# Performance work log

Measured on AMD Instinct MI355X. Metric: run time of the kernel, lower is better.

Reference implementation:

```python
import jax, jax.numpy as jnp
import numpy as np
import math
from jax import lax

D_MODEL = 128
N_HEADS = 8
D_HEAD = D_MODEL // N_HEADS
D_FF = 4 * D_MODEL
KERNEL = 25  # moving_avg kernel size
N_LAYERS = 2
EPS = 1e-5


def moving_avg(x):
    # x: [B, L, D]; replicate-pad (KERNEL-1)//2 at both ends, window mean (AvgPool1d stride 1)
    p = (KERNEL - 1) // 2
    xp = jnp.concatenate([jnp.repeat(x[:, :1], p, axis=1), x, jnp.repeat(x[:, -1:], p, axis=1)], axis=1)
    s = lax.reduce_window(xp, 0.0, lax.add, (1, KERNEL, 1), (1, 1, 1), 'VALID')
    return s / KERNEL


def series_decomp(x):
    mm = moving_avg(x)
    return x - mm, mm


def autocorrelation(q, k, v):
    # q,k,v: [B, L, H, E]; FFT-based period correlation + top-k time-delay aggregation (training path)
    B, L, H, E = q.shape
    top_k = int(1 * math.log(L))  # factor=1
    qf = jnp.fft.rfft(q.transpose(0, 2, 3, 1), axis=-1)
    kf = jnp.fft.rfft(k.transpose(0, 2, 3, 1), axis=-1)
    corr = jnp.fft.irfft(qf * jnp.conj(kf), n=L, axis=-1)  # [B, H, E, L]
    vals = v.transpose(0, 2, 3, 1)                          # [B, H, E, L]
    mean_value = corr.mean(axis=(1, 2))                     # [B, L]
    _, index = lax.top_k(mean_value.mean(axis=0), top_k)    # [top_k], lags shared over batch
    weights = mean_value[:, index]                          # [B, top_k]
    tmp_corr = jax.nn.softmax(weights, axis=-1)
    agg = jnp.zeros_like(vals)
    for i in range(top_k):  # static small loop (top_k = 8)
        pattern = jnp.roll(vals, -index[i], axis=-1)
        agg = agg + pattern * tmp_corr[:, i][:, None, None, None]
    return agg.transpose(0, 3, 1, 2)  # [B, L, H, E]


def attn_layer(x, w, b):
    # w: [4, D, D] (q,k,v,out torch-Linear weights), b: [4, D]
    B, L, D = x.shape
    q = (jnp.einsum('bld,ed->ble', x, w[0]) + b[0]).reshape(B, L, N_HEADS, D_HEAD)
    k = (jnp.einsum('bld,ed->ble', x, w[1]) + b[1]).reshape(B, L, N_HEADS, D_HEAD)
    v = (jnp.einsum('bld,ed->ble', x, w[2]) + b[2]).reshape(B, L, N_HEADS, D_HEAD)
    o = autocorrelation(q, k, v).reshape(B, L, D)
    return jnp.einsum('bld,ed->ble', o, w[3]) + b[3]


def encoder_layer(x, w, b, w1, w2):
    x = x + attn_layer(x, w, b)
    x, _ = series_decomp(x)
    y = jax.nn.gelu(jnp.einsum('bld,fd->blf', x, w1), approximate=False)  # conv1 (k=1, no bias)
    y = jnp.einsum('blf,df->bld', y, w2)                                   # conv2 (k=1, no bias)
    res, _ = series_decomp(x + y)
    return res


def reference(x_enc, emb_w, attn_w, attn_b, ffn_w1, ffn_w2, norm_g, norm_b, fc1_w, fc1_b, fc2_w, fc2_b):
    # token embedding: Conv1d(C -> D, kernel 3, circular padding, no bias)
    xc = x_enc.transpose(0, 2, 1)  # [B, C, L]
    xc = jnp.concatenate([xc[:, :, -1:], xc, xc[:, :, :1]], axis=-1)
    h = lax.conv_general_dilated(xc, emb_w, (1,), 'VALID', dimension_numbers=('NCH', 'OIH', 'NCH'))
    h = h.transpose(0, 2, 1)  # [B, L, D]
    for l in range(N_LAYERS):
        h = encoder_layer(h, attn_w[l], attn_b[l], ffn_w1[l], ffn_w2[l])
    # my_Layernorm: LayerNorm then subtract time-mean
    mu = h.mean(axis=-1, keepdims=True)
    var = ((h - mu) ** 2).mean(axis=-1, keepdims=True)
    ln = (h - mu) / jnp.sqrt(var + EPS) * norm_g + norm_b
    h = ln - ln.mean(axis=1, keepdims=True)
    # head: gelu -> mean pool over time -> MLP
    h = jax.nn.gelu(h, approximate=False).mean(axis=1)  # [B, D]
    h = jax.nn.relu(jnp.einsum('bd,hd->bh', h, fc1_w) + fc1_b)
    return jnp.einsum('bh,ch->bc', h, fc2_w) + fc2_b


def setup_inputs() -> dict:
    key = jax.random.key(0)
    ks = jax.random.split(key, 8)
    B, L, C, NC, FC = 32, 4096, 12, 5, 128
    s = 0.02
    return {
        'x_enc': jax.random.normal(ks[0], (B, L, C), jnp.float32),
        'emb_w': jax.random.normal(ks[1], (D_MODEL, C, 3), jnp.float32) * s,
        'attn_w': jax.random.normal(ks[2], (N_LAYERS, 4, D_MODEL, D_MODEL), jnp.float32) * s,
        'attn_b': jnp.zeros((N_LAYERS, 4, D_MODEL), jnp.float32),
        'ffn_w1': jax.random.normal(ks[3], (N_LAYERS, D_FF, D_MODEL), jnp.float32) * s,
        'ffn_w2': jax.random.normal(ks[4], (N_LAYERS, D_MODEL, D_FF), jnp.float32) * s,
        'norm_g': jnp.ones((D_MODEL,), jnp.float32),
        'norm_b': jnp.zeros((D_MODEL,), jnp.float32),
        'fc1_w': jax.random.normal(ks[5], (FC, D_MODEL), jnp.float32) * s,
        'fc1_b': jnp.zeros((FC,), jnp.float32),
        'fc2_w': jax.random.normal(ks[6], (NC, FC), jnp.float32) * s,
        'fc2_b': jnp.zeros((NC,), jnp.float32),
    }
```

## Files before the change

kernel.cpp:

```cpp
#include <hip/hip_runtime.h>
#include <math.h>

#define L_SEQ 4096
#define BATCH 32
#define DM 128

typedef short short8 __attribute__((ext_vector_type(8)));
typedef float f32x4 __attribute__((ext_vector_type(4)));

__device__ __forceinline__ float gelu_f(float x) {
    return 0.5f * x * (1.0f + erff(x * 0.70710678118654752f));
}
__device__ __forceinline__ float gelu_fast(float x) {
    float ax = fabsf(x);
    if (ax < 1.0f) {
        float z = x * 0.70710678118654752f;
        float z2 = z * z;
        float p = 1.0f + z2 * (-0.333333333f + z2 * (0.1f + z2 * (-0.0238095238f +
                  z2 * (4.62962963e-3f + z2 * (-7.57575758e-4f)))));
        return 0.5f * x * (1.0f + 1.1283791670955126f * z * p);
    }
    return 0.5f * x * (1.0f + erff(x * 0.70710678118654752f));
}
__device__ __forceinline__ unsigned short f2b(float f) {
    unsigned u = __float_as_uint(f);
    u += 0x7fffu + ((u >> 16) & 1u);
    return (unsigned short)(u >> 16);
}
__device__ __forceinline__ float b2f(unsigned short h) {
    return __uint_as_float(((unsigned)h) << 16);
}

__global__ __launch_bounds__(256) void kembed(const float* __restrict__ x,
                                              const float* __restrict__ w,
                                              float* __restrict__ h) {
    __shared__ float xs[130][12];
    __shared__ float wsm[128][37];
    int b = blockIdx.x >> 5;
    int lt = blockIdx.x & 31;
    int l0 = lt * 128;
    int tid = threadIdx.x;
    for (int i = tid; i < 130 * 12; i += 256) {
        int r = i / 12, c = i - r * 12;
        int gl = (l0 - 1 + r + 4096) & 4095;
        xs[r][c] = x[((size_t)b * 4096 + gl) * 12 + c];
    }
    for (int i = tid; i < 128 * 36; i += 256) {
        int o = i / 36, j = i - o * 36;
        wsm[o][j] = w[i];
    }
    __syncthreads();
    int o = tid & 127, lh = tid >> 7;
    float wr[36];
#pragma unroll
    for (int j = 0; j < 36; j++) wr[j] = wsm[o][j];
    int base_r = lh * 64;
    float ring[4][12];
#pragma unroll
    for (int c = 0; c < 12; c++) { ring[0][c] = xs[base_r][c]; ring[1][c] = xs[base_r + 1][c]; }
    float* hp = h + ((size_t)b * 4096 + l0 + lh * 64) * 128 + o;
#pragma unroll 4
    for (int st = 0; st < 64; st++) {
        int s0 = st & 3, s1 = (st + 1) & 3, s2 = (st + 2) & 3;
#pragma unroll
        for (int c = 0; c < 12; c++) ring[s2][c] = xs[base_r + st + 2][c];
        float s = 0.f;
#pragma unroll
        for (int c = 0; c < 12; c++)
            s += wr[c * 3 + 0] * ring[s0][c] + wr[c * 3 + 1] * ring[s1][c] + wr[c * 3 + 2] * ring[s2][c];
        hp[(size_t)st * 128] = s;
    }
}

__global__ __launch_bounds__(256) void kprepw(const float* __restrict__ w1,
                                              const float* __restrict__ w2,
                                              unsigned short* __restrict__ w1img,
                                              unsigned short* __restrict__ w2img) {
    int t = blockIdx.x * 256 + threadIdx.x;
    int layer = t >> 17; int rem = t & 131071;
    if (rem < 65536) {
        int R = rem >> 7, x = rem & 127;
        int g = x >> 3, j = x & 7;
        int srcc = ((g ^ (R & 7)) << 3) + j;
        w1img[(size_t)layer * 65536 + rem] = f2b(w1[(size_t)layer * 65536 + R * 128 + srcc]);
    } else {
        int r2 = rem - 65536;
        int c = r2 >> 13; int D = (r2 >> 6) & 127; int x = r2 & 63;
        int g = x >> 3, j = x & 7;
        int srcf = c * 64 + ((g ^ (D & 7)) << 3) + j;
        w2img[(size_t)layer * 65536 + r2] = f2b(w2[(size_t)layer * 65536 + D * 512 + srcf]);
    }
}

__global__ __launch_bounds__(256, 2) void kgemm_qk3(const float* __restrict__ A,
                                                    const float* __restrict__ aw,
                                                    const float* __restrict__ ab,
                                                    int half, float* __restrict__ CT) {
    __shared__ __align__(16) char smem[65536];
    short* Ah = (short*)smem;
    short* Al = (short*)(smem + 16384);
    short* Wh = (short*)(smem + 32768);
    short* Wl = (short*)(smem + 49152);
    int y = blockIdx.y;
    const float* Wp = aw + (size_t)y * 16384 + (size_t)half * 64 * 128;
    const float* bias = ab + y * 128 + half * 64;
    int row0 = blockIdx.x * 64;
    int tid = threadIdx.x;
#pragma unroll
    for (int u = 0; u < 4; u++) {
        int task = tid + u * 256;
        int r = task >> 4, cg = task & 15;
        int dst = r * 128 + ((cg ^ (r & 7)) << 3);
        const float* src = A + ((size_t)(row0 + r)) * 128 + cg * 8;
        float4 xa = *(const float4*)src, ya = *(const float4*)(src + 4);
        float av[8] = {xa.x, xa.y, xa.z, xa.w, ya.x, ya.y, ya.z, ya.w};
        short8 hi, lo;
#pragma unroll
        for (int j = 0; j < 8; j++) {
            unsigned short h = f2b(av[j]);
            hi[j] = (short)h; lo[j] = (short)f2b(av[j] - b2f(h));
        }
        *(short8*)(Ah + dst) = hi; *(short8*)(Al + dst) = lo;
        const float* wsrc = Wp + (size_t)r * 128 + cg * 8;
        float4 xw = *(const float4*)wsrc, yw = *(const float4*)(wsrc + 4);
        float wv[8] = {xw.x, xw.y, xw.z, xw.w, yw.x, yw.y, yw.z, yw.w};
        short8 whi, wlo;
#pragma unroll
        for (int j = 0; j < 8; j++) {
            unsigned short h = f2b(wv[j]);
            whi[j] = (short)h; wlo[j] = (short)f2b(wv[j] - b2f(h));
        }
        *(short8*)(Wh + dst) = whi; *(short8*)(Wl + dst) = wlo;
    }
    __syncthreads();
    int l = tid & 63; int w = tid >> 6; int wm = w >> 1, wn = w & 1;
    f32x4 acc[2][2];
#pragma unroll
    for (int i = 0; i < 2; i++)
#pragma unroll
        for (int j = 0; j < 2; j++) acc[i][j] = (f32x4){0.f, 0.f, 0.f, 0.f};
#pragma unroll
    for (int ks = 0; ks < 4; ks++) {
        int cg = ks * 4 + (l >> 4);
        short8 ah[2], al2[2], bh[2], bl[2];
#pragma unroll
        for (int mi = 0; mi < 2; mi++) {
            int rm = wm * 32 + mi * 16 + (l & 15);
            int off = rm * 128 + ((cg ^ (rm & 7)) << 3);
            ah[mi] = *(short8*)(Ah + off); al2[mi] = *(short8*)(Al + off);
        }
#pragma unroll
        for (int ni = 0; ni < 2; ni++) {
            int rn = wn * 32 + ni * 16 + (l & 15);
            int off = rn * 128 + ((cg ^ (rn & 7)) << 3);
            bh[ni] = *(short8*)(Wh + off); bl[ni] = *(short8*)(Wl + off);
        }
#pragma unroll
        for (int mi = 0; mi < 2; mi++)
#pragma unroll
            for (int ni = 0; ni < 2; ni++) {
                acc[mi][ni] = __builtin_amdgcn_mfma_f32_16x16x32_bf16(ah[mi], bh[ni], acc[mi][ni], 0, 0, 0);
                acc[mi][ni] = __builtin_amdgcn_mfma_f32_16x16x32_bf16(ah[mi], bl[ni], acc[mi][ni], 0, 0, 0);
                acc[mi][ni] = __builtin_amdgcn_mfma_f32_16x16x32_bf16(al2[mi], bh[ni], acc[mi][ni], 0, 0, 0);
            }
    }
    __syncthreads();
    float* Dsh = (float*)smem;
#pragma unroll
    for (int mi = 0; mi < 2; mi++)
#pragma unroll
        for (int ni = 0; ni < 2; ni++)
#pragma unroll
            for (int rr = 0; rr < 4; rr++) {
                int m = wm * 32 + mi * 16 + (l >> 4) * 4 + rr;
                int n = wn * 32 + ni * 16 + (l & 15);
                Dsh[n * 68 + m] = acc[mi][ni][rr] + bias[n];
            }
    __syncthreads();
    int b = row0 >> 12; int l0 = row0 & 4095;
    int cbase = y * 64;
#pragma unroll
    for (int u = 0; u < 4; u++) {
        int task = tid + u * 256;
        int c = task >> 4, m4 = (task & 15) * 4;
        float4 v = *(float4*)&Dsh[c * 68 + m4];
        *(float4*)&CT[((size_t)(b * 128 + cbase + c)) * 4096 + l0 + m4] = v;
    }
}

template <int AT, int EPI>
__global__ __launch_bounds__(256, 2) void kgemm_mfma(const void* __restrict__ Ap,
                                                     const float* __restrict__ Wf,
                                                     const float* __restrict__ bias,
                                                     const float* __restrict__ res,
                                                     const float* __restrict__ tcb,
                                                     const int* __restrict__ idxb,
                                                     void* __restrict__ outp) {
    __shared__ __align__(16) char smem[65536];
    short* As = (short*)smem;
    short* Ws = (short*)(smem + 32768);
    int tid = threadIdx.x;
    size_t row0 = (size_t)blockIdx.x * 128;
#pragma unroll
    for (int u = 0; u < 8; u++) {
        int g = tid + u * 256;
        int r = g >> 4, cg = g & 15;
        int dsti = r * 128 + ((cg ^ (r & 7)) << 3);
        short8 v;
        if (AT == 0) {
            const float* src = (const float*)Ap + (row0 + r) * 128 + cg * 8;
            float4 x = *(const float4*)src, y = *(const float4*)(src + 4);
            v[0] = f2b(x.x); v[1] = f2b(x.y); v[2] = f2b(x.z); v[3] = f2b(x.w);
            v[4] = f2b(y.x); v[5] = f2b(y.y); v[6] = f2b(y.z); v[7] = f2b(y.w);
        } else if (AT == 1) {
            v = *(const short8*)((const short*)Ap + (row0 + r) * 128 + cg * 8);
        } else {
            const unsigned short* Vb = (const unsigned short*)Ap;
            int b = (int)(row0 >> 12);
            int l0 = (int)(row0 & 4095);
            float accv[8];
#pragma unroll
            for (int j = 0; j < 8; j++) accv[j] = 0.f;
#pragma unroll
            for (int i = 0; i < 8; i++) {
                float wgt = tcb[b * 8 + i];
                int lr = (l0 + r + idxb[i]) & 4095;
                short8 vv = *(const short8*)(Vb + ((size_t)(b * 4096 + lr)) * 128 + cg * 8);
#pragma unroll
                for (int j = 0; j < 8; j++) accv[j] += wgt * b2f((unsigned short)vv[j]);
            }
#pragma unroll
            for (int j = 0; j < 8; j++) v[j] = (short)f2b(accv[j]);
        }
        *(short8*)(As + dsti) = v;
        const float* ws = Wf + (size_t)r * 128 + cg * 8;
        float4 wx = *(const float4*)ws, wy = *(const float4*)(ws + 4);
        short8 wv;
        wv[0] = f2b(wx.x); wv[1] = f2b(wx.y); wv[2] = f2b(wx.z); wv[3] = f2b(wx.w);
        wv[4] = f2b(wy.x); wv[5] = f2b(wy.y); wv[6] = f2b(wy.z); wv[7] = f2b(wy.w);
        *(short8*)(Ws + dsti) = wv;
    }
    __syncthreads();
    int l = tid & 63; int w = tid >> 6; int wm = w >> 1, wn = w & 1;
    f32x4 acc[4][4];
#pragma unroll
    for (int i = 0; i < 4; i++)
#pragma unroll
        for (int j = 0; j < 4; j++) acc[i][j] = (f32x4){0.f, 0.f, 0.f, 0.f};
#pragma unroll
    for (int ks = 0; ks < 4; ks++) {
        int cg = ks * 4 + (l >> 4);
        short8 af[4], bf[4];
#pragma unroll
        for (int mi = 0; mi < 4; mi++) {
            int rm = wm * 64 + mi * 16 + (l & 15);
            af[mi] = *(short8*)(As + rm * 128 + ((cg ^ (rm & 7)) << 3));
        }
#pragma unroll
        for (int ni = 0; ni < 4; ni++) {
            int rn = wn * 64 + ni * 16 + (l & 15);
            bf[ni] = *(short8*)(Ws + rn * 128 + ((cg ^ (rn & 7)) << 3));
        }
#pragma unroll
        for (int mi = 0; mi < 4; mi++)
#pragma unroll
            for (int ni = 0; ni < 4; ni++)
                acc[mi][ni] = __builtin_amdgcn_mfma_f32_16x16x32_bf16(af[mi], bf[ni], acc[mi][ni], 0, 0, 0);
    }
    __syncthreads();
    float* Dsh = (float*)smem;
#pragma unroll
    for (int mi = 0; mi < 4; mi++)
#pragma unroll
        for (int ni = 0; ni < 4; ni++)
#pragma unroll
            for (int rr = 0; rr < 4; rr++)
                Dsh[(wm * 64 + mi * 16 + (l >> 4) * 4 + rr) * 128 + wn * 64 + ni * 16 + (l & 15)] = acc[mi][ni][rr];
    __syncthreads();
#pragma unroll
    for (int u = 0; u < 8; u++) {
        int g = tid + u * 256;
        int r = g >> 4, c8 = (g & 15) * 8;
        float vv[8];
#pragma unroll
        for (int j = 0; j < 8; j++) vv[j] = Dsh[r * 128 + c8 + j] + bias[c8 + j];
        if (EPI == 1) {
            const float* rp = res + (row0 + r) * 128 + c8;
#pragma unroll
            for (int j = 0; j < 8; j++) vv[j] += rp[j];
            float* op = (float*)outp + (row0 + r) * 128 + c8;
            *(float4*)op = make_float4(vv[0], vv[1], vv[2], vv[3]);
            *(float4*)(op + 4) = make_float4(vv[4], vv[5], vv[6], vv[7]);
        } else {
            short8 ov;
#pragma unroll
            for (int j = 0; j < 8; j++) ov[j] = (short)f2b(vv[j]);
            *(short8*)((short*)outp + (row0 + r) * 128 + c8) = ov;
        }
    }
}

__global__ __launch_bounds__(256, 2) void kffn_mfma(const float* __restrict__ xs,
                                                    const unsigned short* __restrict__ w1img,
                                                    const unsigned short* __restrict__ w2img,
                                                    float* __restrict__ outp) {
    __shared__ __align__(16) char smem[81920];
    short* xsl = (short*)smem;
    short* w1t = (short*)(smem + 32768);
    short* tt  = (short*)(smem + 49152);
    short* w2t = (short*)(smem + 65536);
    int tid = threadIdx.x;
    size_t row0 = (size_t)blockIdx.x * 128;
#pragma unroll
    for (int u = 0; u < 8; u++) {
        int g = tid + u * 256;
        int r = g >> 4, cg = g & 15;
        const float* src = xs + (row0 + r) * 128 + cg * 8;
        float4 x = *(const float4*)src, y = *(const float4*)(src + 4);
        short8 v;
        v[0] = f2b(x.x); v[1] = f2b(x.y); v[2] = f2b(x.z); v[3] = f2b(x.w);
        v[4] = f2b(y.x); v[5] = f2b(y.y); v[6] = f2b(y.z); v[7] = f2b(y.w);
        *(short8*)(xsl + r * 128 + ((cg ^ (r & 7)) << 3)) = v;
    }
    int l = tid & 63; int w = tid >> 6; int wm = w >> 1, wn = w & 1;
    f32x4 acc2[4][4];
#pragma unroll
    for (int i = 0; i < 4; i++)
#pragma unroll
        for (int j = 0; j < 4; j++) acc2[i][j] = (f32x4){0.f, 0.f, 0.f, 0.f};
    for (int fb = 0; fb < 8; fb++) {
        __syncthreads();
#pragma unroll
        for (int u = 0; u < 4; u++) {
            int task = tid + u * 256;
            int r = task >> 4, cg = task & 15;
            *(short8*)(w1t + r * 128 + cg * 8) =
                *(const short8*)(w1img + ((size_t)(fb * 64 + r)) * 128 + cg * 8);
            int r2 = task >> 3, cg2 = task & 7;
            *(short8*)(w2t + r2 * 64 + cg2 * 8) =
                *(const short8*)(w2img + ((size_t)(fb * 128 + r2)) * 64 + cg2 * 8);
        }
        __syncthreads();
        f32x4 a1[4][2];
#pragma unroll
        for (int i = 0; i < 4; i++)
#pragma unroll
            for (int j = 0; j < 2; j++) a1[i][j] = (f32x4){0.f, 0.f, 0.f, 0.f};
#pragma unroll
        for (int ks = 0; ks < 4; ks++) {
            int cg = ks * 4 + (l >> 4);
            short8 af[4], bf[2];
#pragma unroll
            for (int mi = 0; mi < 4; mi++) {
                int rm = wm * 64 + mi * 16 + (l & 15);
                af[mi] = *(short8*)(xsl + rm * 128 + ((cg ^ (rm & 7)) << 3));
            }
#pragma unroll
            for (int ni = 0; ni < 2; ni++) {
                int rn = wn * 32 + ni * 16 + (l & 15);
                bf[ni] = *(short8*)(w1t + rn * 128 + ((cg ^ (rn & 7)) << 3));
            }
#pragma unroll
            for (int mi = 0; mi < 4; mi++)
#pragma unroll
                for (int ni = 0; ni < 2; ni++)
                    a1[mi][ni] = __builtin_amdgcn_mfma_f32_16x16x32_bf16(af[mi], bf[ni], a1[mi][ni], 0, 0, 0);
        }
#pragma unroll
        for (int mi = 0; mi < 4; mi++)
#pragma unroll
            for (int ni = 0; ni < 2; ni++)
#pragma unroll
                for (int rr = 0; rr < 4; rr++) {
                    int m = wm * 64 + mi * 16 + (l >> 4) * 4 + rr;
                    int f = wn * 32 + ni * 16 + (l & 15);
                    tt[m * 64 + (((f >> 3) ^ (m & 7)) << 3) + (f & 7)] = (short)f2b(gelu_fast(a1[mi][ni][rr]));
                }
        __syncthreads();
#pragma unroll
        for (int ks = 0; ks < 2; ks++) {
            int cg = ks * 4 + (l >> 4);
            short8 af[4], bf[4];
#pragma unroll
            for (int mi = 0; mi < 4; mi++) {
                int rm = wm * 64 + mi * 16 + (l & 15);
                af[mi] = *(short8*)(tt + rm * 64 + ((cg ^ (rm & 7)) << 3));
            }
#pragma unroll
            for (int ni = 0; ni < 4; ni++) {
                int rn = wn * 64 + ni * 16 + (l & 15);
                bf[ni] = *(short8*)(w2t + rn * 64 + ((cg ^ (rn & 7)) << 3));
            }
#pragma unroll
            for (int mi = 0; mi < 4; mi++)
#pragma unroll
                for (int ni = 0; ni < 4; ni++)
                    acc2[mi][ni] = __builtin_amdgcn_mfma_f32_16x16x32_bf16(af[mi], bf[ni], acc2[mi][ni], 0, 0, 0);
        }
    }
    __syncthreads();
    float* Dsh = (float*)smem;
#pragma unroll
    for (int mi = 0; mi < 4; mi++)
#pragma unroll
        for (int ni = 0; ni < 4; ni++)
#pragma unroll
            for (int rr = 0; rr < 4; rr++)
                Dsh[(wm * 64 + mi * 16 + (l >> 4) * 4 + rr) * 128 + wn * 64 + ni * 16 + (l & 15)] = acc2[mi][ni][rr];
    __syncthreads();
#pragma unroll
    for (int u = 0; u < 8; u++) {
        int g = tid + u * 256;
        int r = g >> 4, c8 = (g & 15) * 8;
        const float* rp = xs + (row0 + r) * 128 + c8;
        float* op = outp + (row0 + r) * 128 + c8;
        float4 o0, o1;
        o0.x = Dsh[r * 128 + c8 + 0] + rp[0]; o0.y = Dsh[r * 128 + c8 + 1] + rp[1];
        o0.z = Dsh[r * 128 + c8 + 2] + rp[2]; o0.w = Dsh[r * 128 + c8 + 3] + rp[3];
        o1.x = Dsh[r * 128 + c8 + 4] + rp[4]; o1.y = Dsh[r * 128 + c8 + 5] + rp[5];
        o1.z = Dsh[r * 128 + c8 + 6] + rp[6]; o1.w = Dsh[r * 128 + c8 + 7] + rp[7];
        *(float4*)op = o0; *(float4*)(op + 4) = o1;
    }
}

#define FIDX(a) ((a) + ((a) >> 4))

__device__ __forceinline__ float2 twget(const float2* __restrict__ tw, int a, float sgn) {
    float2 T = tw[a & 1023];
    int hi = (a >> 10) & 3;
    float cs = (hi & 1) ? ((hi & 2) ? T.y : -T.y) : ((hi & 2) ? -T.x : T.x);
    float sn = (hi & 1) ? ((hi & 2) ? -T.x : T.x) : ((hi & 2) ? -T.y : T.y);
    return make_float2(cs, sn * sgn);
}

__device__ void fft4096_r4(float2* __restrict__ b0, float2* __restrict__ b1,
                           const float2* __restrict__ tw, float sgn, int tid) {
    float2* cur = b0; float2* nxt = b1;
#pragma unroll
    for (int t = 0; t < 6; t++) {
        int s = 1 << (t << 1);
        int q = tid & (s - 1);
        int ps = tid - q;
        float2 a0 = cur[FIDX(tid)];
        float2 a1 = cur[FIDX(tid + 1024)];
        float2 a2 = cur[FIDX(tid + 2048)];
        float2 a3 = cur[FIDX(tid + 3072)];
        float t0x = a0.x + a2.x, t0y = a0.y + a2.y;
        float t1x = a0.x - a2.x, t1y = a0.y - a2.y;
        float t2x = a1.x + a3.x, t2y = a1.y + a3.y;
        float t3x = a1.x - a3.x, t3y = a1.y - a3.y;
        float it3x = -sgn * t3y, it3y = sgn * t3x;
        float2 A0 = make_float2(t0x + t2x, t0y + t2y);
        float2 A1 = make_float2(t1x + it3x, t1y + it3y);
        float2 A2 = make_float2(t0x - t2x, t0y - t2y);
        float2 A3 = make_float2(t1x - it3x, t1y - it3y);
        int ob = q + (ps << 2);
        nxt[FIDX(ob)] = A0;
        float2 w1 = twget(tw, ps, sgn);
        float2 w2 = twget(tw, ps * 2, sgn);
        float2 w3 = twget(tw, ps * 3, sgn);
        nxt[FIDX(ob + s)] = make_float2(A1.x * w1.x - A1.y * w1.y, A1.x * w1.y + A1.y * w1.x);
        nxt[FIDX(ob + 2 * s)] = make_float2(A2.x * w2.x - A2.y * w2.y, A2.x * w2.y + A2.y * w2.x);
        nxt[FIDX(ob + 3 * s)] = make_float2(A3.x * w3.x - A3.y * w3.y, A3.x * w3.y + A3.y * w3.x);
        __syncthreads();
        float2* tp = cur; cur = nxt; nxt = tp;
    }
}

__global__ __launch_bounds__(1024) void kfft_fwd(const float* __restrict__ qkT,
                                                 float* __restrict__ Pws, int ghalf) {
    __shared__ float2 bufA[4352];
    __shared__ float2 bufB[4352];
    __shared__ float2 tw[1024];
    int tid = threadIdx.x;
    {
        float sn, cs;
        sincosf(1.5339807878856412e-3f * (float)tid, &sn, &cs);
        tw[tid] = make_float2(cs, sn);
    }
    int b = blockIdx.x >> 3;
    int gl = blockIdx.x & 7;
    float2 pacc[4];
#pragma unroll
    for (int j = 0; j < 4; j++) pacc[j] = make_float2(0.f, 0.f);
    for (int c8 = 0; c8 < 8; c8++) {
        int c = gl * 8 + c8;
        const float* qrow = qkT + ((size_t)(b * 128 + c)) * 4096;
        const float* krow = qkT + ((size_t)(b * 128 + 64 + c)) * 4096;
        __syncthreads();
#pragma unroll
        for (int j = 0; j < 4; j++) {
            int i = tid + j * 1024;
            bufA[FIDX(i)] = make_float2(qrow[i], krow[i]);
        }
        __syncthreads();
        fft4096_r4(bufA, bufB, tw, -1.f, tid);
#pragma unroll
        for (int j = 0; j < 4; j++) {
            int f = tid + j * 1024;
            float2 Zf = bufA[FIDX(f)];
            float2 Zm = bufA[FIDX((4096 - f) & 4095)];
            float Qre = 0.5f * (Zf.x + Zm.x), Qim = 0.5f * (Zf.y - Zm.y);
            float Kre = 0.5f * (Zf.y + Zm.y), Kim = -0.5f * (Zf.x - Zm.x);
            pacc[j].x += Qre * Kre + Qim * Kim;
            pacc[j].y += Qim * Kre - Qre * Kim;
        }
    }
    float2* P = (float2*)Pws + (size_t)(b * 16 + ghalf * 8 + gl) * 4096;
#pragma unroll
    for (int j = 0; j < 4; j++) { int f = tid + j * 1024; P[f] = pacc[j]; }
}

__global__ __launch_bounds__(1024) void kfft_inv(const float* __restrict__ Pws,
                                                 float* __restrict__ meanv) {
    __shared__ float2 bufA[4352];
    __shared__ float2 bufB[4352];
    __shared__ float2 tw[1024];
    int tid = threadIdx.x;
    {
        float sn, cs;
        sincosf(1.5339807878856412e-3f * (float)tid, &sn, &cs);
        tw[tid] = make_float2(cs, sn);
    }
    int b = blockIdx.x;
    const float2* P = (const float2*)Pws + (size_t)b * 16 * 4096;
#pragma unroll
    for (int j = 0; j < 4; j++) {
        int i = tid + j * 1024;
        float2 s = make_float2(0.f, 0.f);
#pragma unroll
        for (int gg = 0; gg < 16; gg++) { float2 v = P[gg * 4096 + i]; s.x += v.x; s.y += v.y; }
        bufA[FIDX(i)] = s;
    }
    __syncthreads();
    fft4096_r4(bufA, bufB, tw, 1.f, tid);
    const float scale = 1.0f / (4096.0f * 128.0f);
#pragma unroll
    for (int j = 0; j < 4; j++) {
        int i = tid + j * 1024;
        meanv[b * 4096 + i] = bufA[FIDX(i)].x * scale;
    }
}

__global__ __launch_bounds__(256) void ktopk(const float* __restrict__ meanv,
                                             int* __restrict__ idxout,
                                             float* __restrict__ tc) {
    __shared__ float cm[4096];
    __shared__ float rv[256];
    __shared__ int ri[256];
    __shared__ int sidx[8];
    for (int c = threadIdx.x; c < 4096; c += 256) {
        float s = 0.f;
        for (int b = 0; b < 32; b++) s += meanv[b * 4096 + c];
        cm[c] = s;
    }
    __syncthreads();
    for (int it = 0; it < 8; it++) {
        float bv = -1e30f; int bi = 0;
        for (int c = threadIdx.x; c < 4096; c += 256) {
            float v = cm[c];
            if (v > bv) { bv = v; bi = c; }
        }
        rv[threadIdx.x] = bv; ri[threadIdx.x] = bi;
        __syncthreads();
        for (int off = 128; off > 0; off >>= 1) {
            if (threadIdx.x < off) {
                float v2 = rv[threadIdx.x + off]; int i2 = ri[threadIdx.x + off];
                if (v2 > rv[threadIdx.x] || (v2 == rv[threadIdx.x] && i2 < ri[threadIdx.x])) {
                    rv[threadIdx.x] = v2; ri[threadIdx.x] = i2;
                }
            }
            __syncthreads();
        }
        if (threadIdx.x == 0) { sidx[it] = ri[0]; idxout[it] = ri[0]; cm[ri[0]] = -1e30f; }
        __syncthreads();
    }
    if (threadIdx.x < 32) {
        int b = threadIdx.x;
        float w[8]; float mx = -1e30f;
#pragma unroll
        for (int i = 0; i < 8; i++) { w[i] = meanv[b * 4096 + sidx[i]]; mx = fmaxf(mx, w[i]); }
        float s = 0.f;
#pragma unroll
        for (int i = 0; i < 8; i++) { w[i] = expf(w[i] - mx); s += w[i]; }
#pragma unroll
        for (int i = 0; i < 8; i++) tc[b * 8 + i] = w[i] / s;
    }
}

__global__ __launch_bounds__(256) void kdecomp(const float* __restrict__ in,
                                               float* __restrict__ outp) {
    int b = blockIdx.x >> 4; int ch = blockIdx.x & 15;
    int s = threadIdx.x >> 7; int d = threadIdx.x & 127;
    int l0 = ch * 256 + s * 128;
    const float* base = in + ((size_t)b * 4096) * 128 + d;
    float* obase = outp + ((size_t)b * 4096) * 128 + d;
    float S = 0.f;
#pragma unroll
    for (int j = -12; j <= 12; j++) {
        int lj = l0 + j;
        lj = lj < 0 ? 0 : (lj > 4095 ? 4095 : lj);
        S += base[(size_t)lj * 128];
    }
    for (int st = 0; st < 128; st++) {
        int l = l0 + st;
        float c = base[(size_t)l * 128];
        obase[(size_t)l * 128] = c - S * (1.0f / 25.0f);
        int ln = l + 13 > 4095 ? 4095 : l + 13;
        int lo = l - 12 < 0 ? 0 : l - 12;
        S += base[(size_t)ln * 128] - base[(size_t)lo * 128];
    }
}

__global__ __launch_bounds__(256) void kln(float* __restrict__ h,
                                           const float* __restrict__ g,
                                           const float* __restrict__ bb) {
    int wave = threadIdx.x >> 6; int lane = threadIdx.x & 63;
    size_t row = (size_t)blockIdx.x * 4 + wave;
    float* p = h + row * 128;
    float v0 = p[lane], v1 = p[lane + 64];
    float s = v0 + v1, s2 = v0 * v0 + v1 * v1;
#pragma unroll
    for (int off = 32; off; off >>= 1) { s += __shfl_down(s, off); s2 += __shfl_down(s2, off); }
    s = __shfl(s, 0); s2 = __shfl(s2, 0);
    float mu = s * (1.f / 128.f);
    float var = s2 * (1.f / 128.f) - mu * mu;
    float inv = rsqrtf(var + 1e-5f);
    p[lane] = (v0 - mu) * inv * g[lane] + bb[lane];
    p[lane + 64] = (v1 - mu) * inv * g[lane + 64] + bb[lane + 64];
}

__global__ __launch_bounds__(256) void kpart1(const float* __restrict__ h,
                                              float* __restrict__ part) {
    int b = blockIdx.x >> 3, sl = blockIdx.x & 7;
    int d = threadIdx.x & 127, p = threadIdx.x >> 7;
    const float* base = h + ((size_t)b * 4096 + sl * 512) * 128;
    float acc = 0.f;
    for (int l = p; l < 512; l += 2) acc += base[(size_t)l * 128 + d];
    __shared__ float sh[256];
    sh[threadIdx.x] = acc; __syncthreads();
    if (p == 0) part[(size_t)(b * 8 + sl) * 128 + d] = acc + sh[128 + d];
}

__global__ __launch_bounds__(128) void kpart2(const float* __restrict__ part,
                                              float* __restrict__ outm) {
    int b = blockIdx.x; int d = threadIdx.x;
    float s = 0.f;
#pragma unroll
    for (int q = 0; q < 8; q++) s += part[(size_t)(b * 8 + q) * 128 + d];
    outm[b * 128 + d] = s * (1.f / 4096.f);
}

__global__ __launch_bounds__(256) void kgpart1(const float* __restrict__ h,
                                               const float* __restrict__ msum,
                                               float* __restrict__ part) {
    int b = blockIdx.x >> 3, sl = blockIdx.x & 7;
    int d = threadIdx.x & 127, p = threadIdx.x >> 7;
    const float* base = h + ((size_t)b * 4096 + sl * 512) * 128;
    float m = msum[b * 128 + d];
    float acc = 0.f;
    for (int l = p; l < 512; l += 2) acc += gelu_f(base[(size_t)l * 128 + d] - m);
    __shared__ float sh[256];
    sh[threadIdx.x] = acc; __syncthreads();
    if (p == 0) part[(size_t)(b * 8 + sl) * 128 + d] = acc + sh[128 + d];
}

__global__ __launch_bounds__(256) void khead(const float* __restrict__ gmean,
                                             const float* __restrict__ fc1w,
                                             const float* __restrict__ fc1b,
                                             const float* __restrict__ fc2w,
                                             const float* __restrict__ fc2b,
                                             float* __restrict__ outp) {
    __shared__ float h0[32][128];
    __shared__ float h1[32][128];
    int tid = threadIdx.x;
#pragma unroll
    for (int i = 0; i < 16; i++) {
        int e = tid + i * 256;
        h0[e >> 7][e & 127] = gmean[e];
    }
    __syncthreads();
#pragma unroll
    for (int i = 0; i < 16; i++) {
        int e = tid + i * 256; int b = e >> 7, j = e & 127;
        float s = fc1b[j];
        for (int d = 0; d < 128; d++) s += h0[b][d] * fc1w[j * 128 + d];
        h1[b][j] = fmaxf(s, 0.f);
    }
    __syncthreads();
    if (tid < 160) {
        int b = tid / 5, c2 = tid % 5;
        float s = fc2b[c2];
        for (int j = 0; j < 128; j++) s += h1[b][j] * fc2w[c2 * 128 + j];
        outp[b * 5 + c2] = s;
    }
}

extern "C" void kernel_launch(void* const* d_in, const int* in_sizes, int n_in,
                              void* d_out, int out_size, void* d_ws, size_t ws_size,
                              hipStream_t stream) {
    const float* x_enc  = (const float*)d_in[0];
    const float* emb_w  = (const float*)d_in[1];
    const float* attn_w = (const float*)d_in[2];
    const float* attn_b = (const float*)d_in[3];
    const float* ffn_w1 = (const float*)d_in[4];
    const float* ffn_w2 = (const float*)d_in[5];
    const float* norm_g = (const float*)d_in[6];
    const float* norm_b = (const float*)d_in[7];
    const float* fc1_w  = (const float*)d_in[8];
    const float* fc1_b  = (const float*)d_in[9];
    const float* fc2_w  = (const float*)d_in[10];
    const float* fc2_b  = (const float*)d_in[11];
    float* outp = (float*)d_out;

    float* W = (float*)d_ws;
    const size_t RD = (size_t)BATCH * L_SEQ * DM;
    float* buf0  = W;
    float* buf1  = W + RD;
    float* Pws   = W + 2 * RD;
    float* meanv = Pws + (size_t)4194304;
    float* tcb   = meanv + (size_t)131072;
    int*   idxb  = (int*)(tcb + 256);
    float* part  = tcb + 256 + 64;
    float* msum  = part + 32768;
    float* gsum  = msum + 4096;
    unsigned short* w1img = (unsigned short*)(gsum + 4096);
    unsigned short* w2img = w1img + (size_t)2 * 65536;

    kembed<<<1024, 256, 0, stream>>>(x_enc, emb_w, buf0);
    kprepw<<<1024, 256, 0, stream>>>(ffn_w1, ffn_w2, w1img, w2img);

    float* H = buf0;
    float* S = buf1;
    for (int l = 0; l < 2; l++) {
        const float* aw = attn_w + (size_t)l * 4 * 128 * 128;
        const float* ab = attn_b + (size_t)l * 4 * 128;
        for (int half = 0; half < 2; half++) {
            kgemm_qk3<<<dim3(2048, 2), 256, 0, stream>>>(H, aw, ab, half, S);
            kfft_fwd<<<256, 1024, 0, stream>>>(S, Pws, half);
        }
        kfft_inv<<<32, 1024, 0, stream>>>(Pws, meanv);
        ktopk<<<1, 256, 0, stream>>>(meanv, idxb, tcb);
        unsigned short* Vb = (unsigned short*)S;
        kgemm_mfma<0, 0><<<1024, 256, 0, stream>>>(H, aw + 2 * 128 * 128, ab + 256,
                                                   nullptr, nullptr, nullptr, Vb);
        kgemm_mfma<2, 1><<<1024, 256, 0, stream>>>(Vb, aw + 3 * 128 * 128, ab + 384,
                                                   H, tcb, idxb, H);
        kdecomp<<<512, 256, 0, stream>>>(H, S);
        kffn_mfma<<<1024, 256, 0, stream>>>(S, w1img + (size_t)l * 65536,
                                            w2img + (size_t)l * 65536, H);
        kdecomp<<<512, 256, 0, stream>>>(H, S);
        float* t = H; H = S; S = t;
    }

    kln<<<32768, 256, 0, stream>>>(H, norm_g, norm_b);
    kpart1<<<256, 256, 0, stream>>>(H, part);
    kpart2<<<32, 128, 0, stream>>>(part, msum);
    kgpart1<<<256, 256, 0, stream>>>(H, msum, part);
    kpart2<<<32, 128, 0, stream>>>(part, gsum);
    khead<<<1, 256, 0, stream>>>(gsum, fc1_w, fc1_b, fc2_w, fc2_b, outp);
}
```

Before: 1.030 ms.

## Precompute bf16 attention weight images, hoist FFN A fragments, vectorize decomp

The attention Q/K/V/O weights are now converted once, in kprepw, into pre-swizzled bf16 hi/lo images. The GEMM kernels then copy these images straight into shared memory instead of converting fp32 weights in every block. The FFN kernel keeps its input-row fragments in registers, shrinks its LDS footprint by aliasing buffers, and writes the residual output directly from the accumulators instead of staging it through shared memory. kdecomp switches to float4 loads and stores with shorter per-thread runs. The costs are higher register pressure in the FFN kernel, since launch_bounds no longer asks for 2 blocks per CU, and uncoalesced scalar stores in the FFN epilogue.

```diff
diff --git a/kernel.cpp b/kernel.cpp
--- a/kernel.cpp
+++ b/kernel.cpp
@@ -74,26 +74,53 @@
 
 __global__ __launch_bounds__(256) void kprepw(const float* __restrict__ w1,
                                               const float* __restrict__ w2,
+                                              const float* __restrict__ attn_w,
                                               unsigned short* __restrict__ w1img,
-                                              unsigned short* __restrict__ w2img) {
+                                              unsigned short* __restrict__ w2img,
+                                              unsigned short* __restrict__ qkh,
+                                              unsigned short* __restrict__ qkl,
+                                              unsigned short* __restrict__ voimg) {
     int t = blockIdx.x * 256 + threadIdx.x;
-    int layer = t >> 17; int rem = t & 131071;
-    if (rem < 65536) {
-        int R = rem >> 7, x = rem & 127;
+    if (t < 262144) {
+        int layer = t >> 17; int rem = t & 131071;
+        if (rem < 65536) {
+            int R = rem >> 7, x = rem & 127;
+            int g = x >> 3, j = x & 7;
+            int srcc = ((g ^ (R & 7)) << 3) + j;
+            w1img[(size_t)layer * 65536 + rem] = f2b(w1[(size_t)layer * 65536 + R * 128 + srcc]);
+        } else {
+            int r2 = rem - 65536;
+            int c = r2 >> 13; int D = (r2 >> 6) & 127; int x = r2 & 63;
+            int g = x >> 3, j = x & 7;
+            int srcf = c * 64 + ((g ^ (D & 7)) << 3) + j;
+            w2img[(size_t)layer * 65536 + r2] = f2b(w2[(size_t)layer * 65536 + D * 512 + srcf]);
+        }
+    } else if (t < 327680) {
+        int t2 = t - 262144;
+        int layer = t2 >> 15; int rem = t2 & 32767;
+        int y = rem >> 14; int rem2 = rem & 16383;
+        int r64 = rem2 >> 7; int x = rem2 & 127;
+        int r = r64 & 63;
         int g = x >> 3, j = x & 7;
-        int srcc = ((g ^ (R & 7)) << 3) + j;
-        w1img[(size_t)layer * 65536 + rem] = f2b(w1[(size_t)layer * 65536 + R * 128 + srcc]);
+        int srcc = ((g ^ (r & 7)) << 3) + j;
+        float v = attn_w[(size_t)layer * 65536 + y * 16384 + r64 * 128 + srcc];
+        unsigned short hh = f2b(v);
+        qkh[t2] = hh;
+        qkl[t2] = f2b(v - b2f(hh));
     } else {
-        int r2 = rem - 65536;
-        int c = r2 >> 13; int D = (r2 >> 6) & 127; int x = r2 & 63;
+        int t3 = t - 327680;
+        int layer = t3 >> 15; int rem = t3 & 32767;
+        int mat = rem >> 14; int rem2 = rem & 16383;
+        int r = rem2 >> 7; int x = rem2 & 127;
         int g = x >> 3, j = x & 7;
-        int srcf = c * 64 + ((g ^ (D & 7)) << 3) + j;
-        w2img[(size_t)layer * 65536 + r2] = f2b(w2[(size_t)layer * 65536 + D * 512 + srcf]);
+        int srcc = ((g ^ (r & 7)) << 3) + j;
+        voimg[t3] = f2b(attn_w[(size_t)layer * 65536 + (2 + mat) * 16384 + r * 128 + srcc]);
     }
 }
 
 __global__ __launch_bounds__(256, 2) void kgemm_qk3(const float* __restrict__ A,
-                                                    const float* __restrict__ aw,
+                                                    const unsigned short* __restrict__ qkh,
+                                                    const unsigned short* __restrict__ qkl,
                                                     const float* __restrict__ ab,
                                                     int half, float* __restrict__ CT) {
     __shared__ __align__(16) char smem[65536];
@@ -102,7 +129,8 @@
     short* Wh = (short*)(smem + 32768);
     short* Wl = (short*)(smem + 49152);
     int y = blockIdx.y;
-    const float* Wp = aw + (size_t)y * 16384 + (size_t)half * 64 * 128;
+    const unsigned short* wh = qkh + y * 16384 + half * 8192;
+    const unsigned short* wl = qkl + y * 16384 + half * 8192;
     const float* bias = ab + y * 128 + half * 64;
     int row0 = blockIdx.x * 64;
     int tid = threadIdx.x;
@@ -121,16 +149,9 @@
             hi[j] = (short)h; lo[j] = (short)f2b(av[j] - b2f(h));
         }
         *(short8*)(Ah + dst) = hi; *(short8*)(Al + dst) = lo;
-        const float* wsrc = Wp + (size_t)r * 128 + cg * 8;
-        float4 xw = *(const float4*)wsrc, yw = *(const float4*)(wsrc + 4);
-        float wv[8] = {xw.x, xw.y, xw.z, xw.w, yw.x, yw.y, yw.z, yw.w};
-        short8 whi, wlo;
-#pragma unroll
-        for (int j = 0; j < 8; j++) {
-            unsigned short h = f2b(wv[j]);
-            whi[j] = (short)h; wlo[j] = (short)f2b(wv[j] - b2f(h));
-        }
-        *(short8*)(Wh + dst) = whi; *(short8*)(Wl + dst) = wlo;
+        int lin = r * 128 + cg * 8;
+        *(short8*)(Wh + lin) = *(const short8*)(wh + lin);
+        *(short8*)(Wl + lin) = *(const short8*)(wl + lin);
     }
     __syncthreads();
     int l = tid & 63; int w = tid >> 6; int wm = w >> 1, wn = w & 1;
@@ -190,7 +211,7 @@
 
 template <int AT, int EPI>
 __global__ __launch_bounds__(256, 2) void kgemm_mfma(const void* __restrict__ Ap,
-                                                     const float* __restrict__ Wf,
+                                                     const unsigned short* __restrict__ Wimg,
                                                      const float* __restrict__ bias,
                                                      const float* __restrict__ res,
                                                      const float* __restrict__ tcb,
@@ -212,8 +233,6 @@
             float4 x = *(const float4*)src, y = *(const float4*)(src + 4);
             v[0] = f2b(x.x); v[1] = f2b(x.y); v[2] = f2b(x.z); v[3] = f2b(x.w);
             v[4] = f2b(y.x); v[5] = f2b(y.y); v[6] = f2b(y.z); v[7] = f2b(y.w);
-        } else if (AT == 1) {
-            v = *(const short8*)((const short*)Ap + (row0 + r) * 128 + cg * 8);
         } else {
             const unsigned short* Vb = (const unsigned short*)Ap;
             int b = (int)(row0 >> 12);
@@ -233,12 +252,8 @@
             for (int j = 0; j < 8; j++) v[j] = (short)f2b(accv[j]);
         }
         *(short8*)(As + dsti) = v;
-        const float* ws = Wf + (size_t)r * 128 + cg * 8;
-        float4 wx = *(const float4*)ws, wy = *(const float4*)(ws + 4);
-        short8 wv;
-        wv[0] = f2b(wx.x); wv[1] = f2b(wx.y); wv[2] = f2b(wx.z); wv[3] = f2b(wx.w);
-        wv[4] = f2b(wy.x); wv[5] = f2b(wy.y); wv[6] = f2b(wy.z); wv[7] = f2b(wy.w);
-        *(short8*)(Ws + dsti) = wv;
+        int lin = r * 128 + cg * 8;
+        *(short8*)(Ws + lin) = *(const short8*)(Wimg + lin);
     }
     __syncthreads();
     int l = tid & 63; int w = tid >> 6; int wm = w >> 1, wn = w & 1;
@@ -300,15 +315,15 @@
     }
 }
 
-__global__ __launch_bounds__(256, 2) void kffn_mfma(const float* __restrict__ xs,
-                                                    const unsigned short* __restrict__ w1img,
-                                                    const unsigned short* __restrict__ w2img,
-                                                    float* __restrict__ outp) {
-    __shared__ __align__(16) char smem[81920];
+__global__ __launch_bounds__(256) void kffn_mfma(const float* __restrict__ xs,
+                                                 const unsigned short* __restrict__ w1img,
+                                                 const unsigned short* __restrict__ w2img,
+                                                 float* __restrict__ outp) {
+    __shared__ __align__(16) char smem[49152];
     short* xsl = (short*)smem;
+    short* tt  = (short*)smem;
+    short* w2t = (short*)(smem + 16384);
     short* w1t = (short*)(smem + 32768);
-    short* tt  = (short*)(smem + 49152);
-    short* w2t = (short*)(smem + 65536);
     int tid = threadIdx.x;
     size_t row0 = (size_t)blockIdx.x * 128;
 #pragma unroll
@@ -322,14 +337,25 @@
         v[4] = f2b(y.x); v[5] = f2b(y.y); v[6] = f2b(y.z); v[7] = f2b(y.w);
         *(short8*)(xsl + r * 128 + ((cg ^ (r & 7)) << 3)) = v;
     }
+    __syncthreads();
     int l = tid & 63; int w = tid >> 6; int wm = w >> 1, wn = w & 1;
+    short8 xa[4][4];
+#pragma unroll
+    for (int mi = 0; mi < 4; mi++) {
+        int rm = wm * 64 + mi * 16 + (l & 15);
+#pragma unroll
+        for (int ks = 0; ks < 4; ks++) {
+            int cg = ks * 4 + (l >> 4);
+            xa[mi][ks] = *(short8*)(xsl + rm * 128 + ((cg ^ (rm & 7)) << 3));
+        }
+    }
+    __syncthreads();
     f32x4 acc2[4][4];
 #pragma unroll
     for (int i = 0; i < 4; i++)
 #pragma unroll
         for (int j = 0; j < 4; j++) acc2[i][j] = (f32x4){0.f, 0.f, 0.f, 0.f};
     for (int fb = 0; fb < 8; fb++) {
-        __syncthreads();
 #pragma unroll
         for (int u = 0; u < 4; u++) {
             int task = tid + u * 256;
@@ -349,12 +375,7 @@
 #pragma unroll
         for (int ks = 0; ks < 4; ks++) {
             int cg = ks * 4 + (l >> 4);
-            short8 af[4], bf[2];
-#pragma unroll
-            for (int mi = 0; mi < 4; mi++) {
-                int rm = wm * 64 + mi * 16 + (l & 15);
-                af[mi] = *(short8*)(xsl + rm * 128 + ((cg ^ (rm & 7)) << 3));
-            }
+            short8 bf[2];
 #pragma unroll
             for (int ni = 0; ni < 2; ni++) {
                 int rn = wn * 32 + ni * 16 + (l & 15);
@@ -364,7 +385,7 @@
             for (int mi = 0; mi < 4; mi++)
 #pragma unroll
                 for (int ni = 0; ni < 2; ni++)
-                    a1[mi][ni] = __builtin_amdgcn_mfma_f32_16x16x32_bf16(af[mi], bf[ni], a1[mi][ni], 0, 0, 0);
+                    a1[mi][ni] = __builtin_amdgcn_mfma_f32_16x16x32_bf16(xa[mi][ks], bf[ni], a1[mi][ni], 0, 0, 0);
         }
 #pragma unroll
         for (int mi = 0; mi < 4; mi++)
@@ -397,29 +418,20 @@
                 for (int ni = 0; ni < 4; ni++)
                     acc2[mi][ni] = __builtin_amdgcn_mfma_f32_16x16x32_bf16(af[mi], bf[ni], acc2[mi][ni], 0, 0, 0);
         }
-    }
-    __syncthreads();
-    float* Dsh = (float*)smem;
-#pragma unroll
-    for (int mi = 0; mi < 4; mi++)
-#pragma unroll
-        for (int ni = 0; ni < 4; ni++)
-#pragma unroll
-            for (int rr = 0; rr < 4; rr++)
-                Dsh[(wm * 64 + mi * 16 + (l >> 4) * 4 + rr) * 128 + wn * 64 + ni * 16 + (l & 15)] = acc2[mi][ni][rr];
-    __syncthreads();
-#pragma unroll
-    for (int u = 0; u < 8; u++) {
-        int g = tid + u * 256;
-        int r = g >> 4, c8 = (g & 15) * 8;
-        const float* rp = xs + (row0 + r) * 128 + c8;
-        float* op = outp + (row0 + r) * 128 + c8;
-        float4 o0, o1;
-        o0.x = Dsh[r * 128 + c8 + 0] + rp[0]; o0.y = Dsh[r * 128 + c8 + 1] + rp[1];
-        o0.z = Dsh[r * 128 + c8 + 2] + rp[2]; o0.w = Dsh[r * 128 + c8 + 3] + rp[3];
-        o1.x = Dsh[r * 128 + c8 + 4] + rp[4]; o1.y = Dsh[r * 128 + c8 + 5] + rp[5];
-        o1.z = Dsh[r * 128 + c8 + 6] + rp[6]; o1.w = Dsh[r * 128 + c8 + 7] + rp[7];
-        *(float4*)op = o0; *(float4*)(op + 4) = o1;
+        __syncthreads();
+    }
+#pragma unroll
+    for (int mi = 0; mi < 4; mi++) {
+        int rowm = wm * 64 + mi * 16 + (l >> 4) * 4;
+#pragma unroll
+        for (int ni = 0; ni < 4; ni++) {
+            int col = wn * 64 + ni * 16 + (l & 15);
+#pragma unroll
+            for (int rr = 0; rr < 4; rr++) {
+                size_t off = (row0 + rowm + rr) * 128 + col;
+                outp[off] = xs[off] + acc2[mi][ni][rr];
+            }
+        }
     }
 }
 
@@ -590,25 +602,30 @@
 
 __global__ __launch_bounds__(256) void kdecomp(const float* __restrict__ in,
                                                float* __restrict__ outp) {
-    int b = blockIdx.x >> 4; int ch = blockIdx.x & 15;
-    int s = threadIdx.x >> 7; int d = threadIdx.x & 127;
-    int l0 = ch * 256 + s * 128;
-    const float* base = in + ((size_t)b * 4096) * 128 + d;
-    float* obase = outp + ((size_t)b * 4096) * 128 + d;
-    float S = 0.f;
+    int b = blockIdx.x >> 4; int lc = blockIdx.x & 15;
+    int dg = threadIdx.x & 31; int ls = threadIdx.x >> 5;
+    int l0 = lc * 256 + ls * 32;
+    const float* base = in + (size_t)b * 524288 + dg * 4;
+    float* ob = outp + (size_t)b * 524288 + dg * 4;
+    float sx = 0.f, sy = 0.f, sz = 0.f, sw = 0.f;
 #pragma unroll
     for (int j = -12; j <= 12; j++) {
         int lj = l0 + j;
         lj = lj < 0 ? 0 : (lj > 4095 ? 4095 : lj);
-        S += base[(size_t)lj * 128];
-    }
-    for (int st = 0; st < 128; st++) {
+        float4 v = *(const float4*)(base + (size_t)lj * 128);
+        sx += v.x; sy += v.y; sz += v.z; sw += v.w;
+    }
+    for (int st = 0; st < 32; st++) {
         int l = l0 + st;
-        float c = base[(size_t)l * 128];
-        obase[(size_t)l * 128] = c - S * (1.0f / 25.0f);
+        float4 c = *(const float4*)(base + (size_t)l * 128);
+        float4 o = make_float4(c.x - sx * (1.0f / 25.0f), c.y - sy * (1.0f / 25.0f),
+                               c.z - sz * (1.0f / 25.0f), c.w - sw * (1.0f / 25.0f));
+        *(float4*)(ob + (size_t)l * 128) = o;
         int ln = l + 13 > 4095 ? 4095 : l + 13;
-        int lo = l - 12 < 0 ? 0 : l - 12;
-        S += base[(size_t)ln * 128] - base[(size_t)lo * 128];
+        int lo2 = l - 12 < 0 ? 0 : l - 12;
+        float4 vn = *(const float4*)(base + (size_t)ln * 128);
+        float4 vo = *(const float4*)(base + (size_t)lo2 * 128);
+        sx += vn.x - vo.x; sy += vn.y - vo.y; sz += vn.z - vo.z; sw += vn.w - vo.w;
     }
 }
 
@@ -726,25 +743,28 @@
     float* gsum  = msum + 4096;
     unsigned short* w1img = (unsigned short*)(gsum + 4096);
     unsigned short* w2img = w1img + (size_t)2 * 65536;
+    unsigned short* qkh   = w2img + (size_t)2 * 65536;
+    unsigned short* qkl   = qkh + (size_t)65536;
+    unsigned short* voimg = qkl + (size_t)65536;
 
     kembed<<<1024, 256, 0, stream>>>(x_enc, emb_w, buf0);
-    kprepw<<<1024, 256, 0, stream>>>(ffn_w1, ffn_w2, w1img, w2img);
+    kprepw<<<1536, 256, 0, stream>>>(ffn_w1, ffn_w2, attn_w, w1img, w2img, qkh, qkl, voimg);
 
     float* H = buf0;
     float* S = buf1;
     for (int l = 0; l < 2; l++) {
-        const float* aw = attn_w + (size_t)l * 4 * 128 * 128;
         const float* ab = attn_b + (size_t)l * 4 * 128;
         for (int half = 0; half < 2; half++) {
-            kgemm_qk3<<<dim3(2048, 2), 256, 0, stream>>>(H, aw, ab, half, S);
+            kgemm_qk3<<<dim3(2048, 2), 256, 0, stream>>>(H, qkh + (size_t)l * 32768,
+                                                         qkl + (size_t)l * 32768, ab, half, S);
             kfft_fwd<<<256, 1024, 0, stream>>>(S, Pws, half);
         }
         kfft_inv<<<32, 1024, 0, stream>>>(Pws, meanv);
         ktopk<<<1, 256, 0, stream>>>(meanv, idxb, tcb);
         unsigned short* Vb = (unsigned short*)S;
-        kgemm_mfma<0, 0><<<1024, 256, 0, stream>>>(H, aw + 2 * 128 * 128, ab + 256,
+        kgemm_mfma<0, 0><<<1024, 256, 0, stream>>>(H, voimg + (size_t)l * 32768, ab + 256,
                                                    nullptr, nullptr, nullptr, Vb);
-        kgemm_mfma<2, 1><<<1024, 256, 0, stream>>>(Vb, aw + 3 * 128 * 128, ab + 384,
+        kgemm_mfma<2, 1><<<1024, 256, 0, stream>>>(Vb, voimg + (size_t)l * 32768 + 16384, ab + 384,
                                                    H, tcb, idxb, H);
         kdecomp<<<512, 256, 0, stream>>>(H, S);
         kffn_mfma<<<1024, 256, 0, stream>>>(S, w1img + (size_t)l * 65536,
```

Measured after the change: 1.203 ms. 1.17x slower.
